# Kernel optimization log

Hardware: AMD Instinct MI355X
Metric: run time of the kernel (lower is better)

The kernel has to match this reference:

```python
import jax, jax.numpy as jnp
import numpy as np

N, F_IN, E = 20000, 256, 320000
H, C = 8, 128            # conv1 heads, per-head channels
OUT, DH = 1, 128         # output_dim, dense_hidden
G = 64                   # number of graphs
EPS = 1e-5


def setup_inputs() -> dict:
    key = jax.random.key(0)
    ks = jax.random.split(key, 20)
    s = 0.05
    return {
        'x': jax.random.normal(ks[0], (N, F_IN), jnp.float32),
        'edge_index': jax.random.randint(ks[1], (2, E), 0, N, jnp.int64),
        'batch': jnp.sort(jax.random.randint(ks[2], (N,), 0, G, jnp.int64)),
        # conv1 (GATv2, heads=8, concat)
        'w1_l': jax.random.normal(ks[3], (F_IN, H * C), jnp.float32) * s,
        'w1_r': jax.random.normal(ks[4], (F_IN, H * C), jnp.float32) * s,
        'att1': jax.random.normal(ks[5], (H, C), jnp.float32) * s,
        'b1': jnp.zeros((H * C,), jnp.float32),
        # norm1 (BatchNorm over H*C features)
        'g1': jnp.ones((H * C,), jnp.float32),
        'be1': jnp.zeros((H * C,), jnp.float32),
        # conv2 (GATv2, heads=1, concat=False)
        'w2_l': jax.random.normal(ks[6], (H * C, OUT), jnp.float32) * s,
        'w2_r': jax.random.normal(ks[7], (H * C, OUT), jnp.float32) * s,
        'att2': jax.random.normal(ks[8], (1, OUT), jnp.float32) * s,
        'b2': jnp.zeros((OUT,), jnp.float32),
        # norm2
        'g2': jnp.ones((OUT,), jnp.float32),
        'be2': jnp.zeros((OUT,), jnp.float32),
        # MLP head
        'lw1': jax.random.normal(ks[9], (OUT, DH), jnp.float32) * s,
        'lb1': jnp.zeros((DH,), jnp.float32),
        'lw2': jax.random.normal(ks[10], (DH, OUT), jnp.float32) * s,
        'lb2': jnp.zeros((OUT,), jnp.float32),
    }


def gatv2(x, src, dst, wl, wr, att, bias, heads, ch, concat):
    n = x.shape[0]
    xl = (x @ wl).reshape(n, heads, ch)
    xr = (x @ wr).reshape(n, heads, ch)
    # edge-wise GATv2 score: a^T LeakyReLU(x_l[j] + x_r[i]), slope 0.2
    e = jnp.einsum('ehc,hc->eh', jax.nn.leaky_relu(xl[src] + xr[dst], 0.2), att)
    # segment softmax over incoming edges per target node
    emax = jax.ops.segment_max(e, dst, num_segments=n)
    ee = jnp.exp(e - emax[dst])
    denom = jax.ops.segment_sum(ee, dst, num_segments=n)
    alpha = ee / (denom[dst] + 1e-16)
    out = jax.ops.segment_sum(alpha[..., None] * xl[src], dst, num_segments=n)  # [n,h,c]
    if concat:
        return out.reshape(n, heads * ch) + bias
    return out.mean(axis=1) + bias


def batchnorm(x, g, b):
    mu = x.mean(axis=0)
    var = ((x - mu) ** 2).mean(axis=0)
    return (x - mu) * jax.lax.rsqrt(var + EPS) * g + b


def reference(x, edge_index, batch, w1_l, w1_r, att1, b1, g1, be1,
              w2_l, w2_r, att2, b2, g2, be2, lw1, lb1, lw2, lb2):
    n = x.shape[0]
    loops = jnp.arange(n, dtype=edge_index.dtype)
    src = jnp.concatenate([edge_index[0], loops])  # add self-loops (PyG default)
    dst = jnp.concatenate([edge_index[1], loops])

    h = gatv2(x, src, dst, w1_l, w1_r, att1, b1, H, C, concat=True)
    h = jax.nn.leaky_relu(batchnorm(h, g1, be1), 0.01)
    # dropout: eval mode (identity)
    h = gatv2(h, src, dst, w2_l, w2_r, att2, b2, 1, OUT, concat=False)
    h = jax.nn.leaky_relu(batchnorm(h, g2, be2), 0.01)

    # global mean pool over graphs
    sums = jax.ops.segment_sum(h, batch, num_segments=G)
    cnt = jax.ops.segment_sum(jnp.ones((n, 1), h.dtype), batch, num_segments=G)
    pooled = sums / jnp.maximum(cnt, 1.0)

    out = jax.nn.leaky_relu(pooled @ lw1 + lb1, 0.01)
    return out @ lw2 + lb2
```

## Files before the change

### kernel.cpp

```cpp
#include <hip/hip_runtime.h>
#include <hip/hip_bf16.h>


__device__ __forceinline__ float lrelu(float x, float s) { return x > 0.f ? x : s * x; }

typedef _Float16 half8 __attribute__((ext_vector_type(8)));
typedef _Float16 half4v __attribute__((ext_vector_type(4)));
typedef _Float16 half2v __attribute__((ext_vector_type(2)));
typedef float f32x4 __attribute__((ext_vector_type(4)));

#define GLOBAL_AS __attribute__((address_space(1)))
#define LDS_AS __attribute__((address_space(3)))

__device__ __forceinline__ void async_copy16(const void* g, void* l) {
  __builtin_amdgcn_global_load_lds((const GLOBAL_AS unsigned int*)g,
                                   (LDS_AS unsigned int*)l, 16, 0, 0);
}

__global__ void zero_ints(int* __restrict__ p, int n) {
  const int t = blockIdx.x * blockDim.x + threadIdx.x;
  if (t < n) p[t] = 0;
}

__global__ void edge_hist(const int* __restrict__ ei, int E, int N,
                          int* __restrict__ counts) {
  const int t = blockIdx.x * blockDim.x + threadIdx.x;
  if (t >= E + N) return;
  const int dst = (t < E) ? ei[E + t] : (t - E);
  atomicAdd(&counts[dst], 1);
}

__global__ __launch_bounds__(1024) void scan_counts(const int* __restrict__ counts,
                                                    int* __restrict__ row_ptr,
                                                    int* __restrict__ cursor, int N) {
  __shared__ int sdata[1024];
  __shared__ int lcnt[20480];
  const int t = threadIdx.x;
  if (N <= 20480) {
    for (int j = t; j < N; j += 1024) lcnt[j] = counts[j];
    __syncthreads();
    const int chunk = (N + 1023) / 1024;
    const int s0 = min(N, t * chunk);
    const int s1 = min(N, s0 + chunk);
    int lsum = 0;
    for (int i = s0; i < s1; ++i) lsum += lcnt[i];
    sdata[t] = lsum;
    __syncthreads();
    for (int off = 1; off < 1024; off <<= 1) {
      int v = 0;
      if (t >= off) v = sdata[t - off];
      __syncthreads();
      sdata[t] += v;
      __syncthreads();
    }
    int run = sdata[t] - lsum;
    for (int i = s0; i < s1; ++i) { const int c = lcnt[i]; lcnt[i] = run; run += c; }
    if (s0 < N && s1 == N) row_ptr[N] = run;
    __syncthreads();
    for (int j = t; j < N; j += 1024) {
      const int v = lcnt[j];
      row_ptr[j] = v;
      cursor[j] = v;
    }
  } else {
    const int chunk = (N + 1023) / 1024;
    const int s0 = min(N, t * chunk);
    const int s1 = min(N, s0 + chunk);
    int lsum = 0;
    for (int i = s0; i < s1; ++i) lsum += counts[i];
    sdata[t] = lsum;
    __syncthreads();
    for (int off = 1; off < 1024; off <<= 1) {
      int v = 0;
      if (t >= off) v = sdata[t - off];
      __syncthreads();
      sdata[t] += v;
      __syncthreads();
    }
    int run = sdata[t] - lsum;
    for (int i = s0; i < s1; ++i) {
      row_ptr[i] = run;
      cursor[i] = run;
      run += counts[i];
    }
    if (s0 < N && s1 == N) row_ptr[N] = run;
  }
}

__global__ void edge_scatter(const int* __restrict__ ei, int E, int N,
                             int* __restrict__ cursor, int* __restrict__ col) {
  const int t = blockIdx.x * blockDim.x + threadIdx.x;
  if (t >= E + N) return;
  const int dst = (t < E) ? ei[E + t] : (t - E);
  const int src = (t < E) ? ei[t] : (t - E);
  const int pos = atomicAdd(&cursor[dst], 1);
  col[pos] = src;
}

__global__ void convert_x(const float* __restrict__ x, _Float16* __restrict__ A2, int M) {
  const int t = blockIdx.x * blockDim.x + threadIdx.x;
  if (t >= M * 64) return;
  const int m = t >> 6;
  const int k4 = (t & 63) * 4;
  const float4 v = *(const float4*)(x + (size_t)m * 256 + k4);
  const float sx = 16.f;
  *(half4v*)(A2 + (size_t)m * 256 + k4) =
      (half4v){(_Float16)(v.x * sx), (_Float16)(v.y * sx),
               (_Float16)(v.z * sx), (_Float16)(v.w * sx)};
}

__global__ __launch_bounds__(256) void convert_w(const float* __restrict__ wl,
                                                 const float* __restrict__ wr,
                                                 _Float16* __restrict__ B2,
                                                 int colOff, int W) {
  const int n = blockIdx.x;
  const int k = threadIdx.x;
  const float v = 16.f * ((n < W) ? wl[k * 1024 + colOff + n]
                                  : wr[k * 1024 + colOff + (n - W)]);
  B2[(size_t)n * 256 + k] = (_Float16)v;
}

__global__ __launch_bounds__(256) void gemm_mfma(const _Float16* __restrict__ A2,
                                                 const _Float16* __restrict__ B2,
                                                 _Float16* __restrict__ C,
                                                 int M, int Ntot) {
  __shared__ __align__(16) _Float16 LDSbuf[2 * 128 * 64];
  _Float16* As = LDSbuf;
  _Float16* Bs = LDSbuf + 128 * 64;
  const int tid = threadIdx.x;
  const int lane = tid & 63;
  const int wv = tid >> 6;
  const int wm = wv & 1, wn = wv >> 1;
  const int m_blk = blockIdx.y * 128;
  const int n_blk = blockIdx.x * 128;
  const int row16 = lane & 15, quad = lane >> 4;
  f32x4 acc[4][4] = {};

  for (int kt = 0; kt < 4; ++kt) {
    const int kg = kt * 64;
#pragma unroll
    for (int j = 0; j < 4; ++j) {
      const int ci = j * 256 + tid;
      const int row = ci >> 3;
      const int c = ci & 7;
      const int gc = c ^ (row & 7);
      _Float16* ldsA = &As[(j * 256 + wv * 64) * 8];
      _Float16* ldsB = &Bs[(j * 256 + wv * 64) * 8];
      const int growA = min(m_blk + row, M - 1);
      async_copy16(A2 + (size_t)growA * 256 + kg + gc * 8, ldsA);
      async_copy16(B2 + (size_t)(n_blk + row) * 256 + kg + gc * 8, ldsB);
    }
    __syncthreads();
#pragma unroll
    for (int ks = 0; ks < 2; ++ks) {
      half8 af[4], bf[4];
#pragma unroll
      for (int mi = 0; mi < 4; ++mi) {
        const int r = wm * 64 + mi * 16 + row16;
        const int cl = (ks * 4 + quad) ^ (r & 7);
        af[mi] = *(const half8*)&As[r * 64 + cl * 8];
      }
#pragma unroll
      for (int ni = 0; ni < 4; ++ni) {
        const int r = wn * 64 + ni * 16 + row16;
        const int cl = (ks * 4 + quad) ^ (r & 7);
        bf[ni] = *(const half8*)&Bs[r * 64 + cl * 8];
      }
#pragma unroll
      for (int mi = 0; mi < 4; ++mi)
#pragma unroll
        for (int ni = 0; ni < 4; ++ni)
          acc[mi][ni] = __builtin_amdgcn_mfma_f32_16x16x32_f16(af[mi], bf[ni], acc[mi][ni], 0, 0, 0);
    }
    __syncthreads();
  }
  const float inv = 1.f / 256.f;
  _Float16* tw = LDSbuf + wv * 4096;
#pragma unroll
  for (int mi = 0; mi < 4; ++mi)
#pragma unroll
    for (int reg = 0; reg < 4; ++reg) {
      const int r_in = mi * 16 + quad * 4 + reg;
#pragma unroll
      for (int ni = 0; ni < 4; ++ni)
        tw[r_in * 64 + ni * 16 + row16] = (_Float16)(acc[mi][ni][reg] * inv);
    }
#pragma unroll
  for (int p8 = 0; p8 < 8; ++p8) {
    const int row = p8 * 8 + (lane >> 3);
    const int grow = m_blk + wm * 64 + row;
    if (grow < M) {
      const half8 v = *(const half8*)&tw[row * 64 + (lane & 7) * 8];
      *(half8*)(C + (size_t)grow * Ntot + n_blk + wn * 64 + (lane & 7) * 8) = v;
    }
  }
}

__global__ __launch_bounds__(256, 8) void conv1_attn_hw(const _Float16* __restrict__ xlrp,
                                                        const int* __restrict__ row_ptr,
                                                        const int* __restrict__ col,
                                                        const float* __restrict__ att,
                                                        const float* __restrict__ bias,
                                                        _Float16* __restrict__ h1, int N) {
  union H8 { half8 v; half2v p[4]; };
  const int wv = threadIdx.x >> 6;
  const int lane = threadIdx.x & 63;
  const int i = blockIdx.x * 2 + (wv >> 1);
  if (i >= N) return;
  const int f = (wv & 1) * 512 + lane * 8;
  half2v a2[4], xr2[4];
  float acc[8];
#pragma unroll
  for (int p = 0; p < 4; ++p)
    a2[p] = (half2v){(_Float16)att[f + 2 * p], (_Float16)att[f + 2 * p + 1]};
  {
    H8 u;
    u.v = *(const half8*)(xlrp + (size_t)i * 2048 + 1024 + f);
#pragma unroll
    for (int k = 0; k < 4; ++k) xr2[k] = u.p[k];
  }
#pragma unroll
  for (int c = 0; c < 8; ++c) acc[c] = 0.f;
  float m = -3.0e38f, l = 0.f;
  const int kb = row_ptr[i];
  const int ke = row_ptr[i + 1];
  for (int base = kb; base < ke; base += 64) {
    const int cnt = min(64, ke - base);
    const int myc = (lane < cnt) ? col[base + lane] : 0;
    H8 xc, xn;
    {
      const int s0 = __shfl(myc, 0);
      xc.v = *(const half8*)(xlrp + (size_t)s0 * 2048 + f);
    }
    for (int q = 0; q < cnt; ++q) {
      if (q + 1 < cnt) {
        const int sn = __shfl(myc, q + 1);
        xn.v = *(const half8*)(xlrp + (size_t)sn * 2048 + f);
      }
      float s = 0.f;
#pragma unroll
      for (int p = 0; p < 4; ++p) {
        const half2v xp = xc.p[p];
        const half2v t = xp + xr2[p];
        const half2v t5 = t * (half2v){(_Float16)0.2f, (_Float16)0.2f};
        const half2v lr = __builtin_elementwise_max(t, t5);
        s = __builtin_amdgcn_fdot2(a2[p], lr, s, false);
      }
      s += __shfl_xor(s, 8);
      s += __shfl_xor(s, 4);
      s += __shfl_xor(s, 2);
      s += __shfl_xor(s, 1);
      if (s <= m) {
        const float pw = __expf(s - m);
        l += pw;
#pragma unroll
        for (int p = 0; p < 4; ++p) {
          const half2v xp = xc.p[p];
          acc[2 * p] += pw * (float)xp[0];
          acc[2 * p + 1] += pw * (float)xp[1];
        }
      } else {
        const float sc = __expf(m - s);
        m = s;
        l = l * sc + 1.f;
#pragma unroll
        for (int p = 0; p < 4; ++p) {
          const half2v xp = xc.p[p];
          acc[2 * p] = acc[2 * p] * sc + (float)xp[0];
          acc[2 * p + 1] = acc[2 * p + 1] * sc + (float)xp[1];
        }
      }
      xc = xn;
    }
  }
  const float inv = 1.f / (l + 1e-16f);
  H8 u;
#pragma unroll
  for (int k = 0; k < 4; ++k) {
    const int c = 2 * k;
    u.p[k] = (half2v){(_Float16)(acc[c] * inv + bias[f + c]),
                      (_Float16)(acc[c + 1] * inv + bias[f + c + 1])};
  }
  *(half8*)(h1 + (size_t)i * 1024 + f) = u.v;
}

template <int CPT>
__global__ __launch_bounds__(256, 6) void conv1_attn(const _Float16* __restrict__ xlrp,
                                                     const int* __restrict__ row_ptr,
                                                     const int* __restrict__ col,
                                                     const float* __restrict__ att,
                                                     const float* __restrict__ bias,
                                                     _Float16* __restrict__ h1,
                                                     int W, int N) {
  constexpr int PAIRS = CPT / 2;
  constexpr int NV8 = CPT / 8;
  constexpr int HG = 128 / CPT;
  union H8 { half8 v; half2v p[4]; };
  const int lane = threadIdx.x & 63;
  const int i = blockIdx.x * 4 + (threadIdx.x >> 6);
  if (i >= N) return;
  const int f = lane * CPT;
  half2v a2[PAIRS], xr2[PAIRS];
  float acc[CPT];
#pragma unroll
  for (int p = 0; p < PAIRS; ++p)
    a2[p] = (half2v){(_Float16)att[f + 2 * p], (_Float16)att[f + 2 * p + 1]};
  {
    const half8* xrp = (const half8*)(xlrp + (size_t)i * (2 * W) + W + f);
#pragma unroll
    for (int j = 0; j < NV8; ++j) {
      H8 u; u.v = xrp[j];
#pragma unroll
      for (int k = 0; k < 4; ++k) xr2[j * 4 + k] = u.p[k];
    }
  }
#pragma unroll
  for (int c = 0; c < CPT; ++c) acc[c] = 0.f;
  float m = -3.0e38f, l = 0.f;
  const int kb = row_ptr[i];
  const int ke = row_ptr[i + 1];
  for (int base = kb; base < ke; base += 64) {
    const int cnt = min(64, ke - base);
    const int myc = (lane < cnt) ? col[base + lane] : 0;
    H8 xc[NV8], xn[NV8];
    {
      const int s0 = __shfl(myc, 0);
      const half8* rp = (const half8*)(xlrp + (size_t)s0 * (2 * W) + f);
#pragma unroll
      for (int j = 0; j < NV8; ++j) xc[j].v = rp[j];
    }
    for (int q = 0; q < cnt; ++q) {
      if (q + 1 < cnt) {
        const int sn = __shfl(myc, q + 1);
        const half8* rp = (const half8*)(xlrp + (size_t)sn * (2 * W) + f);
#pragma unroll
        for (int j = 0; j < NV8; ++j) xn[j].v = rp[j];
      }
      float s = 0.f;
#pragma unroll
      for (int p = 0; p < PAIRS; ++p) {
        const half2v xp = xc[p >> 2].p[p & 3];
        const half2v t = xp + xr2[p];
        const half2v t5 = t * (half2v){(_Float16)0.2f, (_Float16)0.2f};
        const half2v lr = __builtin_elementwise_max(t, t5);
        s = __builtin_amdgcn_fdot2(a2[p], lr, s, false);
      }
#pragma unroll
      for (int off = HG / 2; off >= 1; off >>= 1) s += __shfl_xor(s, off);
      if (s <= m) {
        const float pw = __expf(s - m);
        l += pw;
#pragma unroll
        for (int p = 0; p < PAIRS; ++p) {
          const half2v xp = xc[p >> 2].p[p & 3];
          acc[2 * p] += pw * (float)xp[0];
          acc[2 * p + 1] += pw * (float)xp[1];
        }
      } else {
        const float sc = __expf(m - s);
        m = s;
        l = l * sc + 1.f;
#pragma unroll
        for (int p = 0; p < PAIRS; ++p) {
          const half2v xp = xc[p >> 2].p[p & 3];
          acc[2 * p] = acc[2 * p] * sc + (float)xp[0];
          acc[2 * p + 1] = acc[2 * p + 1] * sc + (float)xp[1];
        }
      }
#pragma unroll
      for (int j = 0; j < NV8; ++j) xc[j] = xn[j];
    }
  }
  const float inv = 1.f / (l + 1e-16f);
  _Float16* outp = h1 + (size_t)i * 1024 + f;
#pragma unroll
  for (int j = 0; j < NV8; ++j) {
    H8 u;
#pragma unroll
    for (int k = 0; k < 4; ++k) {
      const int c = j * 8 + 2 * k;
      u.p[k] = (half2v){(_Float16)(acc[c] * inv + bias[f + c]),
                        (_Float16)(acc[c + 1] * inv + bias[f + c + 1])};
    }
    ((half8*)outp)[j] = u.v;
  }
}

__global__ __launch_bounds__(256) void bn1_stats(const _Float16* __restrict__ h1,
                                                 float* __restrict__ part, int N) {
  const int f = threadIdx.x * 4;
  const int y = blockIdx.y;
  const int chunk = (N + 255) / 256;
  const int r0 = y * chunk;
  const int r1 = min(N, r0 + chunk);
  float s0 = 0.f, s1 = 0.f, s2 = 0.f, s3 = 0.f;
  float q0 = 0.f, q1 = 0.f, q2 = 0.f, q3 = 0.f;
  for (int r = r0; r < r1; ++r) {
    const half4v v4 = *(const half4v*)(h1 + (size_t)r * 1024 + f);
    const float v0 = (float)v4[0], v1 = (float)v4[1], v2 = (float)v4[2], v3 = (float)v4[3];
    s0 += v0; q0 += v0 * v0;
    s1 += v1; q1 += v1 * v1;
    s2 += v2; q2 += v2 * v2;
    s3 += v3; q3 += v3 * v3;
  }
  float* ps = part + (size_t)y * 1024 + f;
  ps[0] = s0; ps[1] = s1; ps[2] = s2; ps[3] = s3;
  float* pq = part + 262144 + (size_t)y * 1024 + f;
  pq[0] = q0; pq[1] = q1; pq[2] = q2; pq[3] = q3;
}

__global__ __launch_bounds__(256) void bn1_final(const float* __restrict__ part,
                                                 const float* __restrict__ g1,
                                                 const float* __restrict__ be1,
                                                 float* __restrict__ scale1,
                                                 float* __restrict__ shift1, int N) {
  const int c = blockIdx.x * 256 + threadIdx.x;
  float s = 0.f, q = 0.f;
  for (int y = 0; y < 256; ++y) {
    s += part[(size_t)y * 1024 + c];
    q += part[262144 + (size_t)y * 1024 + c];
  }
  const float invN = 1.f / (float)N;
  const float mu = s * invN;
  const float var = q * invN - mu * mu;
  const float rs = 1.f / sqrtf(var + 1e-5f);
  const float sc = rs * g1[c];
  scale1[c] = sc;
  shift1[c] = be1[c] - mu * sc;
}

__global__ __launch_bounds__(256) void bn1_proj(const _Float16* __restrict__ h1,
                                                const float* __restrict__ scale1,
                                                const float* __restrict__ shift1,
                                                const float* __restrict__ w2l,
                                                const float* __restrict__ w2r,
                                                float* __restrict__ xl2,
                                                float* __restrict__ xr2, int N) {
  const int i = blockIdx.x;
  const int tid = threadIdx.x;
  const int f = tid * 4;
  const half4v hv = *(const half4v*)(h1 + (size_t)i * 1024 + f);
  const float4 sc4 = *(const float4*)(scale1 + f);
  const float4 sh4 = *(const float4*)(shift1 + f);
  const float4 wl = *(const float4*)(w2l + f);
  const float4 wr = *(const float4*)(w2r + f);
  float pl = 0.f, pr = 0.f;
  {
    float v;
    v = lrelu((float)hv[0] * sc4.x + sh4.x, 0.01f); pl += v * wl.x; pr += v * wr.x;
    v = lrelu((float)hv[1] * sc4.y + sh4.y, 0.01f); pl += v * wl.y; pr += v * wr.y;
    v = lrelu((float)hv[2] * sc4.z + sh4.z, 0.01f); pl += v * wl.z; pr += v * wr.z;
    v = lrelu((float)hv[3] * sc4.w + sh4.w, 0.01f); pl += v * wl.w; pr += v * wr.w;
  }
#pragma unroll
  for (int off = 32; off; off >>= 1) {
    pl += __shfl_down(pl, off);
    pr += __shfl_down(pr, off);
  }
  __shared__ float sp[8];
  if ((tid & 63) == 0) {
    sp[tid >> 6] = pl;
    sp[4 + (tid >> 6)] = pr;
  }
  __syncthreads();
  if (tid == 0) {
    xl2[i] = sp[0] + sp[1] + sp[2] + sp[3];
    xr2[i] = sp[4] + sp[5] + sp[6] + sp[7];
  }
}

__global__ __launch_bounds__(256) void conv2_attn(const float* __restrict__ xl2,
                                                  const float* __restrict__ xr2,
                                                  const int* __restrict__ row_ptr,
                                                  const int* __restrict__ col,
                                                  const float* __restrict__ att2,
                                                  const float* __restrict__ b2,
                                                  float* __restrict__ out2,
                                                  float* __restrict__ bn2acc, int N) {
  const int i = blockIdx.x * blockDim.x + threadIdx.x;
  float val = 0.f;
  if (i < N) {
    const float a = att2[0];
    const float xr = xr2[i];
    float m = -3.0e38f, l = 0.f, acc = 0.f;
    const int kb = row_ptr[i];
    const int ke = row_ptr[i + 1];
    for (int k = kb; k < ke; ++k) {
      const float xv = xl2[col[k]];
      const float s = a * lrelu(xv + xr, 0.2f);
      const float mn = fmaxf(m, s);
      const float sc = __expf(m - mn);
      const float p = __expf(s - mn);
      l = l * sc + p;
      acc = acc * sc + p * xv;
      m = mn;
    }
    val = acc / (l + 1e-16f) + b2[0];
    out2[i] = val;
  }
  float s = (i < N) ? val : 0.f;
  float q = s * s;
#pragma unroll
  for (int off = 32; off; off >>= 1) {
    s += __shfl_down(s, off);
    q += __shfl_down(q, off);
  }
  __shared__ float red[8];
  if ((threadIdx.x & 63) == 0) {
    red[threadIdx.x >> 6] = s;
    red[4 + (threadIdx.x >> 6)] = q;
  }
  __syncthreads();
  if (threadIdx.x == 0) {
    atomicAdd(&bn2acc[0], red[0] + red[1] + red[2] + red[3]);
    atomicAdd(&bn2acc[1], red[4] + red[5] + red[6] + red[7]);
  }
}

__global__ __launch_bounds__(256) void bn2_pool(const float* __restrict__ out2,
                                                const float* __restrict__ bn2acc,
                                                const float* __restrict__ g2,
                                                const float* __restrict__ be2,
                                                const int* __restrict__ batch,
                                                float* __restrict__ pool_sum,
                                                float* __restrict__ pool_cnt, int N) {
  __shared__ float ls[64];
  __shared__ float lc[64];
  const int tid = threadIdx.x;
  if (tid < 64) { ls[tid] = 0.f; lc[tid] = 0.f; }
  __syncthreads();
  const int i = blockIdx.x * blockDim.x + tid;
  if (i < N) {
    const float invN = 1.f / (float)N;
    const float mu = bn2acc[0] * invN;
    const float var = bn2acc[1] * invN - mu * mu;
    const float rs = 1.f / sqrtf(var + 1e-5f);
    const float v = lrelu((out2[i] - mu) * rs * g2[0] + be2[0], 0.01f);
    const int g = batch[i];
    atomicAdd(&ls[g], v);
    atomicAdd(&lc[g], 1.f);
  }
  __syncthreads();
  if (tid < 64 && lc[tid] != 0.f) {
    atomicAdd(&pool_sum[tid], ls[tid]);
    atomicAdd(&pool_cnt[tid], lc[tid]);
  }
}

__global__ void head_mlp(const float* __restrict__ pool_sum, const float* __restrict__ pool_cnt,
                         const float* __restrict__ lw1, const float* __restrict__ lb1,
                         const float* __restrict__ lw2, const float* __restrict__ lb2,
                         float* __restrict__ out) {
  const int g = threadIdx.x;
  if (g >= 64) return;
  const float p = pool_sum[g] / fmaxf(pool_cnt[g], 1.f);
  float acc = 0.f;
  for (int d = 0; d < 128; ++d) {
    float t = p * lw1[d] + lb1[d];
    t = lrelu(t, 0.01f);
    acc += t * lw2[d];
  }
  out[g] = acc + lb2[0];
}

extern "C" void kernel_launch(void* const* d_in, const int* in_sizes, int n_in,
                              void* d_out, int out_size, void* d_ws, size_t ws_size,
                              hipStream_t stream) {
  const float* x = (const float*)d_in[0];
  const int* ei = (const int*)d_in[1];
  const int* batch = (const int*)d_in[2];
  const float* w1_l = (const float*)d_in[3];
  const float* w1_r = (const float*)d_in[4];
  const float* att1 = (const float*)d_in[5];
  const float* b1 = (const float*)d_in[6];
  const float* g1 = (const float*)d_in[7];
  const float* be1 = (const float*)d_in[8];
  const float* w2_l = (const float*)d_in[9];
  const float* w2_r = (const float*)d_in[10];
  const float* att2 = (const float*)d_in[11];
  const float* b2 = (const float*)d_in[12];
  const float* g2 = (const float*)d_in[13];
  const float* be2 = (const float*)d_in[14];
  const float* lw1 = (const float*)d_in[15];
  const float* lb1 = (const float*)d_in[16];
  const float* lw2 = (const float*)d_in[17];
  const float* lb2 = (const float*)d_in[18];

  const int N = in_sizes[2];
  const int E = in_sizes[1] / 2;
  const int ET = E + N;

  const size_t AL = 255;
  auto al = [&](size_t b) { return (b + AL) & ~AL; };
  const size_t zbytes = (size_t)N * 4 + 4096 + 4096 + 16 + 256 + 256;
  const size_t fixedNoXlr = al((size_t)N * 2048)
                          + 3 * al((size_t)N * 4)
                          + al((size_t)(N + 1) * 4)
                          + al((size_t)ET * 4)
                          + al((size_t)N * 4)
                          + al(zbytes)
                          + al((size_t)524288 * 4)
                          + 2 * al(4096);
  const size_t a2b = al((size_t)N * 256 * 2);
  int P = 1;
  while (P < 8) {
    const size_t xlrb = al((size_t)N * (4096 / P));
    const size_t b2b = al((size_t)(2 * (1024 / P)) * 256 * 2);
    const size_t extra = (P == 1) ? 0 : (a2b + b2b);
    if (fixedNoXlr + xlrb + extra <= ws_size) break;
    P <<= 1;
  }
  const int W = 1024 / P;

  char* ws = (char*)d_ws;
  size_t off = 0;
  auto alloc = [&](size_t b) { size_t p = off; off += al(b); return p; };
  _Float16* h1 = (_Float16*)(ws + alloc((size_t)N * 2048));
  _Float16* xlrp = (_Float16*)(ws + alloc((size_t)N * (4096 / P)));
  float* xl2 = (float*)(ws + alloc((size_t)N * 4));
  float* xr2 = (float*)(ws + alloc((size_t)N * 4));
  float* out2 = (float*)(ws + alloc((size_t)N * 4));
  int* row_ptr = (int*)(ws + alloc((size_t)(N + 1) * 4));
  int* colb = (int*)(ws + alloc((size_t)ET * 4));
  int* cursor = (int*)(ws + alloc((size_t)N * 4));
  char* zbase = ws + alloc(zbytes);
  int* counts = (int*)zbase;
  float* bn2acc = (float*)(zbase + (size_t)N * 4 + 8192);
  float* pool_sum = (float*)(zbase + (size_t)N * 4 + 8192 + 16);
  float* pool_cnt = (float*)(zbase + (size_t)N * 4 + 8192 + 16 + 256);
  float* bn1_part = (float*)(ws + alloc((size_t)524288 * 4));
  float* bn1_scale = (float*)(ws + alloc(4096));
  float* bn1_shift = (float*)(ws + alloc(4096));

  _Float16 *A2, *B2;
  if (P == 1) {
    A2 = (_Float16*)h1;
    B2 = (_Float16*)((char*)h1 + a2b);
  } else {
    A2 = (_Float16*)(ws + alloc((size_t)N * 256 * 2));
    B2 = (_Float16*)(ws + alloc((size_t)(2 * W) * 256 * 2));
  }

  const int zn = (int)(zbytes / 4);
  zero_ints<<<(zn + 255) / 256, 256, 0, stream>>>((int*)zbase, zn);

  edge_hist<<<(ET + 255) / 256, 256, 0, stream>>>(ei, E, N, counts);
  scan_counts<<<1, 1024, 0, stream>>>(counts, row_ptr, cursor, N);
  edge_scatter<<<(ET + 255) / 256, 256, 0, stream>>>(ei, E, N, cursor, colb);

  convert_x<<<(N * 64 + 255) / 256, 256, 0, stream>>>(x, A2, N);
  for (int p = 0; p < P; ++p) {
    convert_w<<<2 * W, 256, 0, stream>>>(w1_l, w1_r, B2, p * W, W);
    gemm_mfma<<<dim3(2 * W / 128, (N + 127) / 128), 256, 0, stream>>>(A2, B2, xlrp, N, 2 * W);
    if (W >= 1024)
      conv1_attn_hw<<<(N + 1) / 2, 256, 0, stream>>>(xlrp, row_ptr, colb,
                                                     att1, b1, h1, N);
    else
      conv1_attn<8><<<(N + 3) / 4, 256, 0, stream>>>(xlrp, row_ptr, colb,
                                                     att1 + p * W, b1 + p * W,
                                                     h1 + p * W, W, N);
  }

  bn1_stats<<<dim3(1, 256), 256, 0, stream>>>(h1, bn1_part, N);
  bn1_final<<<4, 256, 0, stream>>>(bn1_part, g1, be1, bn1_scale, bn1_shift, N);
  bn1_proj<<<N, 256, 0, stream>>>(h1, bn1_scale, bn1_shift, w2_l, w2_r, xl2, xr2, N);
  conv2_attn<<<(N + 255) / 256, 256, 0, stream>>>(xl2, xr2, row_ptr, colb, att2, b2,
                                                  out2, bn2acc, N);
  bn2_pool<<<(N + 255) / 256, 256, 0, stream>>>(out2, bn2acc, g2, be2, batch, pool_sum, pool_cnt, N);
  head_mlp<<<1, 64, 0, stream>>>(pool_sum, pool_cnt, lw1, lb1, lw2, lb2, (float*)d_out);
}
```

Baseline: 370.4 us.

## Fuse CSR build into one grid-barrier kernel, merge converts, swizzle GEMM tiles

Replaces the three CSR kernels (histogram, single-block scan, scatter) with one 64-block kernel that uses atomic-counter grid barriers and a distributed block scan. It also merges the x and weight fp16 conversions into one launch when P==1. The GEMM block index is remapped so consecutive blocks spread across XCD-sized M chunks, aiming for better L2 locality. The changes cut launch count and the serial single-block scan, at the cost of spin barriers that assume all 64 blocks are co-resident.

```diff
diff --git a/kernel.cpp b/kernel.cpp
--- a/kernel.cpp
+++ b/kernel.cpp
@@ -22,83 +22,83 @@
   if (t < n) p[t] = 0;
 }
 
-__global__ void edge_hist(const int* __restrict__ ei, int E, int N,
-                          int* __restrict__ counts) {
-  const int t = blockIdx.x * blockDim.x + threadIdx.x;
-  if (t >= E + N) return;
-  const int dst = (t < E) ? ei[E + t] : (t - E);
-  atomicAdd(&counts[dst], 1);
-}
-
-__global__ __launch_bounds__(1024) void scan_counts(const int* __restrict__ counts,
-                                                    int* __restrict__ row_ptr,
-                                                    int* __restrict__ cursor, int N) {
-  __shared__ int sdata[1024];
-  __shared__ int lcnt[20480];
-  const int t = threadIdx.x;
-  if (N <= 20480) {
-    for (int j = t; j < N; j += 1024) lcnt[j] = counts[j];
+__device__ __forceinline__ void gbar(int* ctr, int nb) {
+  __syncthreads();
+  if (threadIdx.x == 0) {
+    __threadfence();
+    atomicAdd(ctr, 1);
+    while (atomicAdd(ctr, 0) < nb) {
+    }
+    __threadfence();
+  }
+  __syncthreads();
+}
+
+__global__ __launch_bounds__(1024) void csr_build(const int* __restrict__ ei, int E, int N,
+                                                  int* __restrict__ counts,
+                                                  int* __restrict__ row_ptr,
+                                                  int* __restrict__ cursor,
+                                                  int* __restrict__ col,
+                                                  int* __restrict__ bars,
+                                                  int* __restrict__ bsum) {
+  const int nb = gridDim.x;
+  const int b = blockIdx.x, t = threadIdx.x;
+  const int ET = E + N;
+  for (int i = b * 1024 + t; i < ET; i += nb * 1024) {
+    const int dst = (i < E) ? ei[E + i] : (i - E);
+    atomicAdd(&counts[dst], 1);
+  }
+  gbar(&bars[0], nb);
+  const int chunk = (N + nb - 1) / nb;
+  const int c0 = min(N, b * chunk), c1 = min(N, c0 + chunk);
+  const int n_loc = c1 - c0;
+  __shared__ int sv[1024];
+  __shared__ int sred[16];
+  __shared__ int soff;
+  const int myv = (t < n_loc) ? counts[c0 + t] : 0;
+  sv[t] = myv;
+  int r = myv;
+#pragma unroll
+  for (int off = 32; off; off >>= 1) r += __shfl_down(r, off);
+  if ((t & 63) == 0) sred[t >> 6] = r;
+  __syncthreads();
+  if (t == 0) {
+    int s = 0;
+    for (int w = 0; w < 16; ++w) s += sred[w];
+    bsum[b] = s;
+  }
+  gbar(&bars[1], nb);
+  if (t < 64) {
+    int v = (t < b) ? bsum[t] : 0;
+#pragma unroll
+    for (int off = 32; off; off >>= 1) v += __shfl_down(v, off);
+    if (t == 0) soff = v;
+  }
+  __syncthreads();
+  for (int off = 1; off < n_loc; off <<= 1) {
+    const int add = (t >= off && t < n_loc) ? sv[t - off] : 0;
     __syncthreads();
-    const int chunk = (N + 1023) / 1024;
-    const int s0 = min(N, t * chunk);
-    const int s1 = min(N, s0 + chunk);
-    int lsum = 0;
-    for (int i = s0; i < s1; ++i) lsum += lcnt[i];
-    sdata[t] = lsum;
+    if (t < n_loc) sv[t] += add;
     __syncthreads();
-    for (int off = 1; off < 1024; off <<= 1) {
-      int v = 0;
-      if (t >= off) v = sdata[t - off];
-      __syncthreads();
-      sdata[t] += v;
-      __syncthreads();
-    }
-    int run = sdata[t] - lsum;
-    for (int i = s0; i < s1; ++i) { const int c = lcnt[i]; lcnt[i] = run; run += c; }
-    if (s0 < N && s1 == N) row_ptr[N] = run;
-    __syncthreads();
-    for (int j = t; j < N; j += 1024) {
-      const int v = lcnt[j];
-      row_ptr[j] = v;
-      cursor[j] = v;
-    }
-  } else {
-    const int chunk = (N + 1023) / 1024;
-    const int s0 = min(N, t * chunk);
-    const int s1 = min(N, s0 + chunk);
-    int lsum = 0;
-    for (int i = s0; i < s1; ++i) lsum += counts[i];
-    sdata[t] = lsum;
-    __syncthreads();
-    for (int off = 1; off < 1024; off <<= 1) {
-      int v = 0;
-      if (t >= off) v = sdata[t - off];
-      __syncthreads();
-      sdata[t] += v;
-      __syncthreads();
-    }
-    int run = sdata[t] - lsum;
-    for (int i = s0; i < s1; ++i) {
-      row_ptr[i] = run;
-      cursor[i] = run;
-      run += counts[i];
-    }
-    if (s0 < N && s1 == N) row_ptr[N] = run;
-  }
-}
-
-__global__ void edge_scatter(const int* __restrict__ ei, int E, int N,
-                             int* __restrict__ cursor, int* __restrict__ col) {
-  const int t = blockIdx.x * blockDim.x + threadIdx.x;
-  if (t >= E + N) return;
-  const int dst = (t < E) ? ei[E + t] : (t - E);
-  const int src = (t < E) ? ei[t] : (t - E);
-  const int pos = atomicAdd(&cursor[dst], 1);
-  col[pos] = src;
-}
-
-__global__ void convert_x(const float* __restrict__ x, _Float16* __restrict__ A2, int M) {
-  const int t = blockIdx.x * blockDim.x + threadIdx.x;
+  }
+  if (t < n_loc) {
+    const int excl = soff + sv[t] - myv;
+    row_ptr[c0 + t] = excl;
+    cursor[c0 + t] = excl;
+  }
+  if (b == nb - 1 && t == 0) row_ptr[N] = soff + bsum[b];
+  gbar(&bars[2], nb);
+  for (int i = b * 1024 + t; i < ET; i += nb * 1024) {
+    const int dst = (i < E) ? ei[E + i] : (i - E);
+    const int src = (i < E) ? ei[i] : (i - E);
+    const int pos = atomicAdd(&cursor[dst], 1);
+    col[pos] = src;
+  }
+}
+
+__device__ __forceinline__ void convert_x_body(const float* __restrict__ x,
+                                               _Float16* __restrict__ A2,
+                                               int t, int M) {
   if (t >= M * 64) return;
   const int m = t >> 6;
   const int k4 = (t & 63) * 4;
@@ -109,15 +109,37 @@
                (_Float16)(v.z * sx), (_Float16)(v.w * sx)};
 }
 
+__device__ __forceinline__ void convert_w_body(const float* __restrict__ wl,
+                                               const float* __restrict__ wr,
+                                               _Float16* __restrict__ B2,
+                                               int n, int k, int colOff, int W) {
+  const float v = 16.f * ((n < W) ? wl[k * 1024 + colOff + n]
+                                  : wr[k * 1024 + colOff + (n - W)]);
+  B2[(size_t)n * 256 + k] = (_Float16)v;
+}
+
+__global__ __launch_bounds__(256) void convert_xw(const float* __restrict__ x,
+                                                  const float* __restrict__ wl,
+                                                  const float* __restrict__ wr,
+                                                  _Float16* __restrict__ A2,
+                                                  _Float16* __restrict__ B2,
+                                                  int M, int colOff, int W, int nxb) {
+  if ((int)blockIdx.x < nxb) {
+    convert_x_body(x, A2, blockIdx.x * 256 + threadIdx.x, M);
+  } else {
+    convert_w_body(wl, wr, B2, blockIdx.x - nxb, threadIdx.x, colOff, W);
+  }
+}
+
+__global__ void convert_x(const float* __restrict__ x, _Float16* __restrict__ A2, int M) {
+  convert_x_body(x, A2, blockIdx.x * blockDim.x + threadIdx.x, M);
+}
+
 __global__ __launch_bounds__(256) void convert_w(const float* __restrict__ wl,
                                                  const float* __restrict__ wr,
                                                  _Float16* __restrict__ B2,
                                                  int colOff, int W) {
-  const int n = blockIdx.x;
-  const int k = threadIdx.x;
-  const float v = 16.f * ((n < W) ? wl[k * 1024 + colOff + n]
-                                  : wr[k * 1024 + colOff + (n - W)]);
-  B2[(size_t)n * 256 + k] = (_Float16)v;
+  convert_w_body(wl, wr, B2, blockIdx.x, threadIdx.x, colOff, W);
 }
 
 __global__ __launch_bounds__(256) void gemm_mfma(const _Float16* __restrict__ A2,
@@ -127,12 +149,20 @@
   __shared__ __align__(16) _Float16 LDSbuf[2 * 128 * 64];
   _Float16* As = LDSbuf;
   _Float16* Bs = LDSbuf + 128 * 64;
+  const int nt = gridDim.x;
+  const int mt = (M + 127) >> 7;
+  const int mchunk = (mt + 7) >> 3;
+  const int l = blockIdx.y * nt + blockIdx.x;
+  const int k = l >> 3;
+  const int yt = (l & 7) * mchunk + k / nt;
+  if (yt >= mt) return;
+  const int xt = k % nt;
   const int tid = threadIdx.x;
   const int lane = tid & 63;
   const int wv = tid >> 6;
   const int wm = wv & 1, wn = wv >> 1;
-  const int m_blk = blockIdx.y * 128;
-  const int n_blk = blockIdx.x * 128;
+  const int m_blk = yt * 128;
+  const int n_blk = xt * 128;
   const int row16 = lane & 15, quad = lane >> 4;
   f32x4 acc[4][4] = {};
 
@@ -625,6 +655,8 @@
   int* cursor = (int*)(ws + alloc((size_t)N * 4));
   char* zbase = ws + alloc(zbytes);
   int* counts = (int*)zbase;
+  int* bars = (int*)(zbase + (size_t)N * 4);
+  int* bsum = (int*)(zbase + (size_t)N * 4 + 128);
   float* bn2acc = (float*)(zbase + (size_t)N * 4 + 8192);
   float* pool_sum = (float*)(zbase + (size_t)N * 4 + 8192 + 16);
   float* pool_cnt = (float*)(zbase + (size_t)N * 4 + 8192 + 16 + 256);
@@ -644,14 +676,20 @@
   const int zn = (int)(zbytes / 4);
   zero_ints<<<(zn + 255) / 256, 256, 0, stream>>>((int*)zbase, zn);
 
-  edge_hist<<<(ET + 255) / 256, 256, 0, stream>>>(ei, E, N, counts);
-  scan_counts<<<1, 1024, 0, stream>>>(counts, row_ptr, cursor, N);
-  edge_scatter<<<(ET + 255) / 256, 256, 0, stream>>>(ei, E, N, cursor, colb);
-
-  convert_x<<<(N * 64 + 255) / 256, 256, 0, stream>>>(x, A2, N);
+  csr_build<<<64, 1024, 0, stream>>>(ei, E, N, counts, row_ptr, cursor, colb, bars, bsum);
+
+  const int nxb = (N * 64 + 255) / 256;
+  if (P == 1) {
+    convert_xw<<<nxb + 2 * W, 256, 0, stream>>>(x, w1_l, w1_r, A2, B2, N, 0, W, nxb);
+  } else {
+    convert_x<<<nxb, 256, 0, stream>>>(x, A2, N);
+  }
   for (int p = 0; p < P; ++p) {
-    convert_w<<<2 * W, 256, 0, stream>>>(w1_l, w1_r, B2, p * W, W);
-    gemm_mfma<<<dim3(2 * W / 128, (N + 127) / 128), 256, 0, stream>>>(A2, B2, xlrp, N, 2 * W);
+    if (P > 1) convert_w<<<2 * W, 256, 0, stream>>>(w1_l, w1_r, B2, p * W, W);
+    const int nt = 2 * W / 128;
+    const int mt = (N + 127) / 128;
+    const int mchunk = (mt + 7) / 8;
+    gemm_mfma<<<dim3(nt, 8 * mchunk), 256, 0, stream>>>(A2, B2, xlrp, N, 2 * W);
     if (W >= 1024)
       conv1_attn_hw<<<(N + 1) / 2, 256, 0, stream>>>(xlrp, row_ptr, colb,
                                                      att1, b1, h1, N);
```

After: 374.7 us. About the same (+1.2%).
